# Kernel optimization log

Measured on AMD Instinct MI355X. Metric: run time of the kernel, lower is better.

The kernel has to match this reference:

```python
import jax, jax.numpy as jnp
import numpy as np

QP = 127.0          # 2**(8-1)-1, signed symmetric int8
MIN_RANGE = 1e-6


def _ste_round(x):
    # round_pass: forward round, straight-through gradient
    return x + jax.lax.stop_gradient(jnp.round(x) - x)


def _quant_per_tensor(x):
    # symmetric per-tensor: scale = max|x| / Qp (grad flows through max as in source)
    scale = jnp.maximum(jnp.max(jnp.abs(x)), MIN_RANGE) / QP
    return _ste_round(x / scale), scale


def _qlinear(x2d, w, b):
    # faithful to _quantize_global (prefix_token_num=None path):
    #   out = (x_q @ w_q.T + bias) * (s_w * s_x)
    xq, sx = _quant_per_tensor(x2d)
    wq, sw = _quant_per_tensor(w)
    out = jnp.matmul(xq, wq.T) + b[None, :]
    return out * (sw * sx)


def setup_inputs() -> dict:
    key = jax.random.key(0)
    k = jax.random.split(key, 5)
    B, N, D, H = 8, 1024, 1024, 4096
    return {
        "x": jax.random.normal(k[0], (B, N, D), dtype=jnp.float32),
        "w1": jax.random.normal(k[1], (H, D), dtype=jnp.float32) * 0.02,
        "b1": jax.random.normal(k[2], (H,), dtype=jnp.float32) * 0.02,
        "w2": jax.random.normal(k[3], (D, H), dtype=jnp.float32) * 0.02,
        "b2": jax.random.normal(k[4], (D,), dtype=jnp.float32) * 0.02,
    }


def reference(x, w1, b1, w2, b2):
    B, N, D = x.shape
    h = _qlinear(x.reshape(-1, D), w1, b1)          # [B*N, H]
    h = jax.nn.gelu(h, approximate=False)            # exact GELU (nn.GELU default)
    o = _qlinear(h, w2, b2)                          # [B*N, D]
    return o.reshape(B, N, -1)
```

## Files before the change

kernel.cpp:

```cpp
#include <hip/hip_runtime.h>
#include <hip/hip_fp16.h>
#include <cstdint>
#include <cmath>

#define QP    127.0f
#define MINR  1e-6f

#define MTOK 8192
#define DDIM 1024
#define HDIM 4096

typedef __attribute__((ext_vector_type(4))) int int32x4;
typedef __attribute__((ext_vector_type(8))) short short8;

__device__ __forceinline__ void gload16(const void* g, void* l) {
    __builtin_amdgcn_global_load_lds(
        (const __attribute__((address_space(1))) void*)g,
        (__attribute__((address_space(3))) void*)l, 16, 0, 0);
}

__global__ void zero_scales_kernel(float* g) {
    if (threadIdx.x < 4) g[threadIdx.x] = 0.0f;
}

__device__ __forceinline__ float wave_block_max(float m) {
    #pragma unroll
    for (int off = 32; off; off >>= 1) m = fmaxf(m, __shfl_down(m, off));
    __shared__ float sm[4];
    int lane = threadIdx.x & 63, w = threadIdx.x >> 6;
    if (lane == 0) sm[w] = m;
    __syncthreads();
    float bm = 0.0f;
    if (threadIdx.x == 0) bm = fmaxf(fmaxf(sm[0], sm[1]), fmaxf(sm[2], sm[3]));
    return bm;
}

__device__ __forceinline__ void absmax_range(const float4* in4, int n4, int bid, int nb,
                                             float* gout) {
    int tid = bid * blockDim.x + threadIdx.x;
    int stride = nb * blockDim.x;
    float m = 0.0f;
    for (int i = tid; i < n4; i += stride) {
        float4 v = in4[i];
        m = fmaxf(m, fmaxf(fmaxf(fabsf(v.x), fabsf(v.y)), fmaxf(fabsf(v.z), fabsf(v.w))));
    }
    float bm = wave_block_max(m);
    if (threadIdx.x == 0) atomicMax((int*)gout, __float_as_int(bm));
}

__global__ void absmax3_kernel(const float* __restrict__ x, const float* __restrict__ w1,
                               const float* __restrict__ w2, float* __restrict__ gmax) {
    int b = blockIdx.x;
    if (b < 1024)      absmax_range((const float4*)x,  MTOK * DDIM / 4, b,        1024, gmax + 0);
    else if (b < 1536) absmax_range((const float4*)w1, HDIM * DDIM / 4, b - 1024,  512, gmax + 1);
    else               absmax_range((const float4*)w2, DDIM * HDIM / 4, b - 1536,  512, gmax + 3);
}

__device__ __forceinline__ void quant_range(const float4* in4, int* out4, int n4,
                                            int bid, int nb, const float* gm) {
    const float s = fmaxf(*gm, MINR) / QP;
    int tid = bid * blockDim.x + threadIdx.x;
    int stride = nb * blockDim.x;
    for (int i = tid; i < n4; i += stride) {
        float4 v = in4[i];
        int q0 = ((int)rintf(v.x / s)) & 255;
        int q1 = ((int)rintf(v.y / s)) & 255;
        int q2 = ((int)rintf(v.z / s)) & 255;
        int q3 = ((int)rintf(v.w / s)) & 255;
        out4[i] = q0 | (q1 << 8) | (q2 << 16) | (q3 << 24);
    }
}

__global__ void quant3_kernel(const float* __restrict__ x, const float* __restrict__ w1,
                              const float* __restrict__ w2, int8_t* __restrict__ xq,
                              int8_t* __restrict__ w1q, int8_t* __restrict__ w2q,
                              const float* __restrict__ gmax) {
    int b = blockIdx.x;
    if (b < 2048)      quant_range((const float4*)x,  (int*)xq,  MTOK * DDIM / 4, b,        2048, gmax + 0);
    else if (b < 3072) quant_range((const float4*)w1, (int*)w1q, HDIM * DDIM / 4, b - 2048, 1024, gmax + 1);
    else               quant_range((const float4*)w2, (int*)w2q, DDIM * HDIM / 4, b - 3072, 1024, gmax + 3);
}

__global__ void quant_h_kernel(const __half* __restrict__ h, int8_t* __restrict__ hq,
                               const float* __restrict__ gm) {
    const float s = fmaxf(*gm, MINR) / QP;
    const short8* in8 = (const short8*)h;
    int2* out8 = (int2*)hq;
    const int n8 = MTOK * HDIM / 8;
    int tid = blockIdx.x * blockDim.x + threadIdx.x;
    int stride = gridDim.x * blockDim.x;
    for (int i = tid; i < n8; i += stride) {
        short8 v = in8[i];
        int q[8];
        #pragma unroll
        for (int j = 0; j < 8; ++j) {
            __half_raw r; r.x = (unsigned short)v[j];
            float f = __half2float(__half(r));
            q[j] = ((int)rintf(f / s)) & 255;
        }
        int2 o;
        o.x = q[0] | (q[1] << 8) | (q[2] << 16) | (q[3] << 24);
        o.y = q[4] | (q[5] << 8) | (q[6] << 16) | (q[7] << 24);
        out8[i] = o;
    }
}

template<int KD, int ND, bool GELU_EPI, typename OUTT>
__global__ __launch_bounds__(256, 2)
void gemm_i8_kernel(const int8_t* __restrict__ A, const int8_t* __restrict__ B,
                    const float* __restrict__ bias,
                    const float* __restrict__ gmA, const float* __restrict__ gmB,
                    OUTT* __restrict__ out, float* __restrict__ omax) {
    constexpr int NBC = ND / 128;
    __shared__ int8_t lA[128 * 128];
    __shared__ int8_t lB[128 * 128];
    const int t = threadIdx.x;
    const int lane = t & 63;
    const int w = t >> 6;
    const int wm = (w >> 1) * 64;
    const int wn = (w & 1) * 64;
    const int lr = lane & 15;
    const int lg = lane >> 4;

    const int chunk = gridDim.x >> 3;
    const int logical = (blockIdx.x & 7) * chunk + (blockIdx.x >> 3);
    const int bc = logical % NBC;
    const int br = logical / NBC;

    const int8_t* Ab = A + (size_t)br * 128 * KD;
    const int8_t* Bb = B + (size_t)bc * 128 * KD;

    int32x4 acc[4][4] = {};

    for (int kt = 0; kt < KD / 128; ++kt) {
        #pragma unroll
        for (int i = 0; i < 4; ++i) {
            int c = t + i * 256;
            gload16(Ab + (size_t)(c >> 3) * KD + kt * 128 + (c & 7) * 16, &lA[c * 16]);
        }
        #pragma unroll
        for (int i = 0; i < 4; ++i) {
            int c = t + i * 256;
            gload16(Bb + (size_t)(c >> 3) * KD + kt * 128 + (c & 7) * 16, &lB[c * 16]);
        }
        __syncthreads();

        #pragma unroll
        for (int kk = 0; kk < 2; ++kk) {
            int32x4 af[4], bf[4];
            #pragma unroll
            for (int m = 0; m < 4; ++m)
                af[m] = *(const int32x4*)&lA[(wm + m * 16 + lr) * 128 + (kk * 4 + lg) * 16];
            #pragma unroll
            for (int n = 0; n < 4; ++n)
                bf[n] = *(const int32x4*)&lB[(wn + n * 16 + lr) * 128 + (kk * 4 + lg) * 16];
            #pragma unroll
            for (int m = 0; m < 4; ++m)
                #pragma unroll
                for (int n = 0; n < 4; ++n)
                    acc[m][n] = __builtin_amdgcn_mfma_i32_16x16x64_i8(af[m], bf[n], acc[m][n], 0, 0, 0);
        }
        __syncthreads();
    }

    const float sA = fmaxf(*gmA, MINR) / QP;
    const float sB = fmaxf(*gmB, MINR) / QP;
    const float s = sB * sA;
    float lmax = 0.0f;
    #pragma unroll
    for (int m = 0; m < 4; ++m) {
        #pragma unroll
        for (int n = 0; n < 4; ++n) {
            #pragma unroll
            for (int r = 0; r < 4; ++r) {
                int row = br * 128 + wm + m * 16 + lg * 4 + r;
                int col = bc * 128 + wn + n * 16 + lr;
                float f = (float)acc[m][n][r] + bias[col];
                f *= s;
                if (GELU_EPI) {
                    float gg = f * (erff(f / 1.41421356237309504880f) + 1.0f) * 0.5f;
                    out[(size_t)row * ND + col] = (OUTT)gg;
                    lmax = fmaxf(lmax, fabsf(gg));
                } else {
                    out[(size_t)row * ND + col] = (OUTT)f;
                }
            }
        }
    }
    if (GELU_EPI) {
        #pragma unroll
        for (int off = 32; off; off >>= 1) lmax = fmaxf(lmax, __shfl_down(lmax, off));
        __shared__ float red[4];
        if (lane == 0) red[w] = lmax;
        __syncthreads();
        if (t == 0) {
            float bm = fmaxf(fmaxf(red[0], red[1]), fmaxf(red[2], red[3]));
            atomicMax((int*)omax, __float_as_int(bm));
        }
    }
}

extern "C" void kernel_launch(void* const* d_in, const int* in_sizes, int n_in,
                              void* d_out, int out_size, void* d_ws, size_t ws_size,
                              hipStream_t stream) {
    const float* x  = (const float*)d_in[0];
    const float* w1 = (const float*)d_in[1];
    const float* b1 = (const float*)d_in[2];
    const float* w2 = (const float*)d_in[3];
    const float* b2 = (const float*)d_in[4];
    float* out = (float*)d_out;

    uint8_t* ws = (uint8_t*)d_ws;
    float*  gmax = (float*)ws;
    int8_t* xq   = (int8_t*)(ws + 256);
    int8_t* w1q  = xq  + (size_t)MTOK * DDIM;
    int8_t* w2q  = w1q + (size_t)HDIM * DDIM;
    int8_t* hq   = w2q + (size_t)DDIM * HDIM;
    __half* h    = (__half*)(hq + (size_t)MTOK * HDIM);

    zero_scales_kernel<<<1, 64, 0, stream>>>(gmax);

    absmax3_kernel<<<2048, 256, 0, stream>>>(x, w1, w2, gmax);
    quant3_kernel<<<4096, 256, 0, stream>>>(x, w1, w2, xq, w1q, w2q, gmax);

    gemm_i8_kernel<DDIM, HDIM, true, __half>
        <<<2048, 256, 0, stream>>>(xq, w1q, b1, gmax + 0, gmax + 1, h, gmax + 2);

    quant_h_kernel<<<2048, 256, 0, stream>>>(h, hq, gmax + 2);

    gemm_i8_kernel<HDIM, DDIM, false, float>
        <<<512, 256, 0, stream>>>(hq, w2q, b2, gmax + 2, gmax + 3, out, nullptr);
}
```

Baseline: 203.5 us.

## Double-buffer int8 GEMM tiles via register staging with XOR-swizzled LDS

Replaces the direct global-to-LDS loads in both int8 GEMMs with register-staged loads into two LDS buffers, so the next K tile is fetched while the current one feeds MFMA. The LDS layout is XOR-swizzled on 16-byte groups by row to cut bank conflicts on the fragment reads. This doubles LDS use to 64 KB per block, which may limit occupancy to the two blocks per CU given in the launch bounds, and it adds register pressure for the staged tiles.

```diff
diff --git a/kernel.cpp b/kernel.cpp
--- a/kernel.cpp
+++ b/kernel.cpp
@@ -12,12 +12,6 @@
 
 typedef __attribute__((ext_vector_type(4))) int int32x4;
 typedef __attribute__((ext_vector_type(8))) short short8;
-
-__device__ __forceinline__ void gload16(const void* g, void* l) {
-    __builtin_amdgcn_global_load_lds(
-        (const __attribute__((address_space(1))) void*)g,
-        (__attribute__((address_space(3))) void*)l, 16, 0, 0);
-}
 
 __global__ void zero_scales_kernel(float* g) {
     if (threadIdx.x < 4) g[threadIdx.x] = 0.0f;
@@ -107,13 +101,14 @@
 
 template<int KD, int ND, bool GELU_EPI, typename OUTT>
 __global__ __launch_bounds__(256, 2)
-void gemm_i8_kernel(const int8_t* __restrict__ A, const int8_t* __restrict__ B,
+void gemm_rs_kernel(const int8_t* __restrict__ A, const int8_t* __restrict__ B,
                     const float* __restrict__ bias,
                     const float* __restrict__ gmA, const float* __restrict__ gmB,
                     OUTT* __restrict__ out, float* __restrict__ omax) {
+    constexpr int KT = KD / 128;
     constexpr int NBC = ND / 128;
-    __shared__ int8_t lA[128 * 128];
-    __shared__ int8_t lB[128 * 128];
+    __shared__ int8_t lA[2 * 128 * 128];
+    __shared__ int8_t lB[2 * 128 * 128];
     const int t = threadIdx.x;
     const int lane = t & 63;
     const int w = t >> 6;
@@ -122,8 +117,8 @@
     const int lr = lane & 15;
     const int lg = lane >> 4;
 
-    const int chunk = gridDim.x >> 3;
-    const int logical = (blockIdx.x & 7) * chunk + (blockIdx.x >> 3);
+    const int chunkX = gridDim.x >> 3;
+    const int logical = (blockIdx.x & 7) * chunkX + (blockIdx.x >> 3);
     const int bc = logical % NBC;
     const int br = logical / NBC;
 
@@ -131,37 +126,59 @@
     const int8_t* Bb = B + (size_t)bc * 128 * KD;
 
     int32x4 acc[4][4] = {};
-
-    for (int kt = 0; kt < KD / 128; ++kt) {
-        #pragma unroll
-        for (int i = 0; i < 4; ++i) {
-            int c = t + i * 256;
-            gload16(Ab + (size_t)(c >> 3) * KD + kt * 128 + (c & 7) * 16, &lA[c * 16]);
-        }
-        #pragma unroll
-        for (int i = 0; i < 4; ++i) {
-            int c = t + i * 256;
-            gload16(Bb + (size_t)(c >> 3) * KD + kt * 128 + (c & 7) * 16, &lB[c * 16]);
-        }
+    int32x4 ra[4], rb[4];
+
+#define LOADR(kt_) do {                                                           \
+        _Pragma("unroll") for (int i_ = 0; i_ < 4; ++i_) {                        \
+            int c_ = t + i_ * 256;                                                \
+            ra[i_] = *(const int32x4*)(Ab + (size_t)(c_ >> 3) * KD + (kt_) * 128 + (c_ & 7) * 16); \
+            rb[i_] = *(const int32x4*)(Bb + (size_t)(c_ >> 3) * KD + (kt_) * 128 + (c_ & 7) * 16); \
+        } } while (0)
+
+#define WRITE(S) do {                                                             \
+        _Pragma("unroll") for (int i_ = 0; i_ < 4; ++i_) {                        \
+            int c_ = t + i_ * 256;                                                \
+            int r_ = c_ >> 3;                                                     \
+            int d_ = r_ * 128 + (((c_ & 7) ^ (r_ & 7)) << 4);                     \
+            *(int32x4*)&lA[(S) * 16384 + d_] = ra[i_];                            \
+            *(int32x4*)&lB[(S) * 16384 + d_] = rb[i_];                            \
+        } } while (0)
+
+#define COMPUTE(S) do {                                                           \
+        _Pragma("unroll") for (int kk = 0; kk < 2; ++kk) {                        \
+            int32x4 af[4], bf[4];                                                 \
+            _Pragma("unroll") for (int m = 0; m < 4; ++m) {                       \
+                int r_ = wm + m * 16 + lr;                                        \
+                int g_ = kk * 4 + lg;                                             \
+                af[m] = *(const int32x4*)&lA[(S) * 16384 + r_ * 128 + ((g_ ^ (r_ & 7)) << 4)]; \
+            }                                                                     \
+            _Pragma("unroll") for (int n = 0; n < 4; ++n) {                       \
+                int r_ = wn + n * 16 + lr;                                        \
+                int g_ = kk * 4 + lg;                                             \
+                bf[n] = *(const int32x4*)&lB[(S) * 16384 + r_ * 128 + ((g_ ^ (r_ & 7)) << 4)]; \
+            }                                                                     \
+            _Pragma("unroll") for (int m = 0; m < 4; ++m)                         \
+                _Pragma("unroll") for (int n = 0; n < 4; ++n)                     \
+                    acc[m][n] = __builtin_amdgcn_mfma_i32_16x16x64_i8(af[m], bf[n], acc[m][n], 0, 0, 0); \
+        } } while (0)
+
+    LOADR(0);
+    WRITE(0);
+    __syncthreads();
+
+    for (int kt = 0; kt < KT; kt += 2) {
+        if (kt + 1 < KT) LOADR(kt + 1);
+        COMPUTE(0);
+        if (kt + 1 < KT) WRITE(1);
         __syncthreads();
-
-        #pragma unroll
-        for (int kk = 0; kk < 2; ++kk) {
-            int32x4 af[4], bf[4];
-            #pragma unroll
-            for (int m = 0; m < 4; ++m)
-                af[m] = *(const int32x4*)&lA[(wm + m * 16 + lr) * 128 + (kk * 4 + lg) * 16];
-            #pragma unroll
-            for (int n = 0; n < 4; ++n)
-                bf[n] = *(const int32x4*)&lB[(wn + n * 16 + lr) * 128 + (kk * 4 + lg) * 16];
-            #pragma unroll
-            for (int m = 0; m < 4; ++m)
-                #pragma unroll
-                for (int n = 0; n < 4; ++n)
-                    acc[m][n] = __builtin_amdgcn_mfma_i32_16x16x64_i8(af[m], bf[n], acc[m][n], 0, 0, 0);
-        }
+        if (kt + 2 < KT) LOADR(kt + 2);
+        COMPUTE(1);
+        if (kt + 2 < KT) WRITE(0);
         __syncthreads();
     }
+#undef LOADR
+#undef WRITE
+#undef COMPUTE
 
     const float sA = fmaxf(*gmA, MINR) / QP;
     const float sB = fmaxf(*gmB, MINR) / QP;
@@ -223,11 +240,11 @@
     absmax3_kernel<<<2048, 256, 0, stream>>>(x, w1, w2, gmax);
     quant3_kernel<<<4096, 256, 0, stream>>>(x, w1, w2, xq, w1q, w2q, gmax);
 
-    gemm_i8_kernel<DDIM, HDIM, true, __half>
+    gemm_rs_kernel<DDIM, HDIM, true, __half>
         <<<2048, 256, 0, stream>>>(xq, w1q, b1, gmax + 0, gmax + 1, h, gmax + 2);
 
     quant_h_kernel<<<2048, 256, 0, stream>>>(h, hq, gmax + 2);
 
-    gemm_i8_kernel<HDIM, DDIM, false, float>
+    gemm_rs_kernel<HDIM, DDIM, false, float>
         <<<512, 256, 0, stream>>>(hq, w2q, b2, gmax + 2, gmax + 3, out, nullptr);
 }
```

Measured after the change: 212.2 us. 1.04x slower.
